# Kernel optimization log

Measured on AMD Instinct MI355X. Metric: run time of the kernel, lower is better.

## Reference

```python
import jax, jax.numpy as jnp
import numpy as np
import itertools

F = 20        # field_size
D = 16        # embedding_size / output_dims
H = 2         # num_hash
NB = 500000   # num_buckets
B = 4096      # batch
NI = F * (F - 1) // 2  # 190 pairwise interactions


def _interact_indexes(field_size):
    # For each field i, indices of the C(F,2) combinations that contain i -> [F, F-1]
    combos = list(itertools.combinations(range(field_size), 2))
    idx = [[j for j, c in enumerate(combos) if i in c] for i in range(field_size)]
    return np.asarray(idx, dtype=np.int32)


def setup_inputs() -> dict:
    key = jax.random.key(0)
    k0, k1, k2, k3, k4, k5 = jax.random.split(key, 6)
    return {
        "origin_embeddings": jax.random.normal(k0, (B, F, D), jnp.float32),
        "codebook": jax.random.normal(k1, (NB, D), jnp.float32) * 0.01,
        "W_transform": jax.random.normal(k2, (H * D, D), jnp.float32) * 0.05,
        "senet_w1": jax.random.normal(k3, (F * D, F * D), jnp.float32) * 0.02,
        "senet_w2": jax.random.normal(k4, (F * D, NI), jnp.float32) * 0.02,
        # Precomputed hash bucket ids (stands in for the StrongHash of string tokens)
        "hash_idx": jax.random.randint(k5, (H, B, NI), 0, NB, dtype=jnp.int32),
        "interact_indexes": jnp.asarray(_interact_indexes(F)),
    }


def reference(origin_embeddings, codebook, W_transform, senet_w1, senet_w2, hash_idx, interact_indexes):
    b = origin_embeddings.shape[0]
    # multi-hash codebook gathers (hash-share: one codebook): [H, B, NI, D]
    gathered = codebook[hash_idx]
    # merge_mode='concat' over hash functions -> [B, NI, H*D]
    emb = jnp.concatenate([gathered[i] for i in range(gathered.shape[0])], axis=-1)
    # hash_merge_final_transform: Dense(output_dims, no bias) -> [B, NI, D]
    emb = jnp.einsum('bne,ed->bnd', emb, W_transform)
    # SENET (bit squeeze, ratio 1.0, vector excitation, no activation) over origin embeddings
    z = origin_embeddings.reshape(b, -1)          # [B, F*D]
    w = (z @ senet_w1) @ senet_w2                 # [B, NI]
    # gather each field's interactions and weighted-sum ('senetsum')
    field_emb = emb[:, interact_indexes]          # [B, F, F-1, D]
    field_w = w[:, interact_indexes][..., None]   # [B, F, F-1, 1]
    out = jnp.sum(field_emb * field_w, axis=-2)   # [B, F, D]
    return out
```

## Files before the change

### kernel.cpp

```cpp
#include <hip/hip_runtime.h>

#define FF 20
#define NI 190
#define NIP 192
#define BB 4096
#define FD 320

__global__ __launch_bounds__(192) void k_w12(const float* __restrict__ w1,
                                             const float* __restrict__ w2,
                                             float* __restrict__ W12p) {
    __shared__ float srow[FD];
    int r = blockIdx.x;
    for (int j = threadIdx.x; j < FD; j += 192) srow[j] = w1[r * FD + j];
    __syncthreads();
    int c = threadIdx.x;
    float acc = 0.f;
    if (c < NI) {
        for (int k = 0; k < FD; ++k) acc += srow[k] * w2[k * NI + c];
    }
    W12p[r * NIP + c] = acc;
}

__global__ __launch_bounds__(256) void k_w(const float* __restrict__ z,
                                           const float* __restrict__ W12p,
                                           float* __restrict__ wout) {
    __shared__ float zT[32][68];
    __shared__ float Ws[32][64];
    int b0 = blockIdx.x * 64;
    int c0 = blockIdx.y * 64;
    int t = threadIdx.x;
    int tr = t >> 4, tc = t & 15;
    float acc[4][4];
#pragma unroll
    for (int i = 0; i < 4; ++i)
#pragma unroll
        for (int j = 0; j < 4; ++j) acc[i][j] = 0.f;

    for (int k0 = 0; k0 < FD; k0 += 32) {
#pragma unroll
        for (int s = 0; s < 2; ++s) {
            int task = t + s * 256;
            int row = task >> 3, ch = task & 7;
            float4 v = *(const float4*)&z[(b0 + row) * FD + k0 + ch * 4];
            zT[ch * 4 + 0][row] = v.x;
            zT[ch * 4 + 1][row] = v.y;
            zT[ch * 4 + 2][row] = v.z;
            zT[ch * 4 + 3][row] = v.w;
        }
#pragma unroll
        for (int s = 0; s < 2; ++s) {
            int task = t + s * 256;
            int kr = task >> 4, cq = task & 15;
            *(float4*)&Ws[kr][cq * 4] = *(const float4*)&W12p[(k0 + kr) * NIP + c0 + cq * 4];
        }
        __syncthreads();
#pragma unroll
        for (int k = 0; k < 32; ++k) {
            float4 zb = *(const float4*)&zT[k][tr * 4];
            float4 wv = *(const float4*)&Ws[k][tc * 4];
            float zz[4] = {zb.x, zb.y, zb.z, zb.w};
            float ww[4] = {wv.x, wv.y, wv.z, wv.w};
#pragma unroll
            for (int i = 0; i < 4; ++i)
#pragma unroll
                for (int j = 0; j < 4; ++j) acc[i][j] += zz[i] * ww[j];
        }
        __syncthreads();
    }
#pragma unroll
    for (int i = 0; i < 4; ++i) {
        float4 v = make_float4(acc[i][0], acc[i][1], acc[i][2], acc[i][3]);
        *(float4*)&wout[(b0 + tr * 4 + i) * NIP + c0 + tc * 4] = v;
    }
}

#define SA(f, h, d) ((f) * 33 + (h) * 16 + (d))
__global__ __launch_bounds__(320) void k_main(const float* __restrict__ cb,
                                              const float* __restrict__ Wt,
                                              const int* __restrict__ hidx,
                                              const int* __restrict__ iidx,
                                              const float* __restrict__ wbuf,
                                              float* __restrict__ out) {
    __shared__ int s_i0[NI], s_i1[NI];
    __shared__ float s_w[NI];
    __shared__ int s_plist[FF * 19];
    __shared__ float s_W[32 * 16];
    __shared__ float s_acc[19 * 33 + 2 * 16 + 16];

    int t = threadIdx.x;
    int b = blockIdx.x;

    if (t < NI) {
        s_i0[t] = hidx[b * NI + t];
        s_i1[t] = hidx[(BB + b) * NI + t];
        s_w[t] = wbuf[b * NIP + t];
    }
    for (int j = t; j < FF * 19; j += 320) s_plist[j] = iidx[j];
    for (int j = t; j < 512; j += 320) s_W[j] = Wt[j];
    __syncthreads();

    int f = t >> 4, d = t & 15;
    const int* pl = &s_plist[f * 19];
    float a0 = 0.f, a1 = 0.f;
#pragma unroll
    for (int j = 0; j < 19; ++j) {
        int p = pl[j];
        float wv = s_w[p];
        a0 += wv * cb[s_i0[p] * 16 + d];
        a1 += wv * cb[s_i1[p] * 16 + d];
    }
    s_acc[SA(f, 0, d)] = a0;
    s_acc[SA(f, 1, d)] = a1;
    __syncthreads();

    float r = 0.f;
#pragma unroll
    for (int k = 0; k < 16; ++k) {
        r += s_acc[SA(f, 0, k)] * s_W[k * 16 + d];
        r += s_acc[SA(f, 1, k)] * s_W[(16 + k) * 16 + d];
    }
    out[b * FD + t] = r;
}

extern "C" void kernel_launch(void* const* d_in, const int* in_sizes, int n_in,
                              void* d_out, int out_size, void* d_ws, size_t ws_size,
                              hipStream_t stream) {
    const float* origin = (const float*)d_in[0];
    const float* cb     = (const float*)d_in[1];
    const float* Wt     = (const float*)d_in[2];
    const float* w1     = (const float*)d_in[3];
    const float* w2     = (const float*)d_in[4];
    const int*   hidx   = (const int*)d_in[5];
    const int*   iidx   = (const int*)d_in[6];
    float* out = (float*)d_out;

    float* W12p = (float*)d_ws;
    float* wbuf = W12p + FD * NIP;

    k_w12<<<FD, 192, 0, stream>>>(w1, w2, W12p);
    dim3 gw(BB / 64, 3);
    k_w<<<gw, 256, 0, stream>>>(origin, W12p, wbuf);
    k_main<<<BB, 320, 0, stream>>>(cb, Wt, hidx, iidx, wbuf, out);
}
```

Measured before the change: 144.8 us.

## Process four batch rows per block with float4 codebook gathers

Each block of the main kernel now handles four batch rows, and each thread covers one quarter of a field's 16-wide embedding. Codebook rows are read as float4, so the per-element gather turns into vectorised 16-byte loads. The transform matmul reads W from shared memory as float4 and stores its output as float4. This cuts the number of gather instructions and amortises the per-block setup (interaction list, W) over more rows, at the cost of fewer blocks and lower thread-level parallelism per row.

```diff
diff --git a/kernel.cpp b/kernel.cpp
--- a/kernel.cpp
+++ b/kernel.cpp
@@ -5,6 +5,7 @@
 #define NIP 192
 #define BB 4096
 #define FD 320
+#define BPB 4
 
 __global__ __launch_bounds__(192) void k_w12(const float* __restrict__ w1,
                                              const float* __restrict__ w2,
@@ -74,52 +75,75 @@
     }
 }
 
-#define SA(f, h, d) ((f) * 33 + (h) * 16 + (d))
-__global__ __launch_bounds__(320) void k_main(const float* __restrict__ cb,
-                                              const float* __restrict__ Wt,
-                                              const int* __restrict__ hidx,
-                                              const int* __restrict__ iidx,
-                                              const float* __restrict__ wbuf,
-                                              float* __restrict__ out) {
-    __shared__ int s_i0[NI], s_i1[NI];
-    __shared__ float s_w[NI];
+#define SAC(bl, f, h, k) ((((bl) * FF + (f)) * 2 + (h)) * 17 + (k))
+__global__ __launch_bounds__(320, 4) void k_main(const float* __restrict__ cb,
+                                                 const float* __restrict__ Wt,
+                                                 const int* __restrict__ hidx,
+                                                 const int* __restrict__ iidx,
+                                                 const float* __restrict__ wbuf,
+                                                 float* __restrict__ out) {
+    __shared__ int s_i0[BPB][NI], s_i1[BPB][NI];
+    __shared__ float s_w[BPB][NI];
     __shared__ int s_plist[FF * 19];
     __shared__ float s_W[32 * 16];
-    __shared__ float s_acc[19 * 33 + 2 * 16 + 16];
+    __shared__ float s_acc[SAC(BPB - 1, FF - 1, 1, 16) + 1];
 
     int t = threadIdx.x;
-    int b = blockIdx.x;
+    int b0 = blockIdx.x * BPB;
 
-    if (t < NI) {
-        s_i0[t] = hidx[b * NI + t];
-        s_i1[t] = hidx[(BB + b) * NI + t];
-        s_w[t] = wbuf[b * NIP + t];
+#pragma unroll
+    for (int bl = 0; bl < BPB; ++bl) {
+        if (t < NI) {
+            s_i0[bl][t] = hidx[(b0 + bl) * NI + t];
+            s_i1[bl][t] = hidx[(BB + b0 + bl) * NI + t];
+            s_w[bl][t] = wbuf[(b0 + bl) * NIP + t];
+        }
     }
     for (int j = t; j < FF * 19; j += 320) s_plist[j] = iidx[j];
     for (int j = t; j < 512; j += 320) s_W[j] = Wt[j];
     __syncthreads();
 
-    int f = t >> 4, d = t & 15;
+    int bl = t / 80;
+    int r = t % 80;
+    int f = r >> 2, dq = r & 3;
+
+    const float4* cb4 = (const float4*)cb;
     const int* pl = &s_plist[f * 19];
-    float a0 = 0.f, a1 = 0.f;
+    float4 a0 = make_float4(0.f, 0.f, 0.f, 0.f);
+    float4 a1 = make_float4(0.f, 0.f, 0.f, 0.f);
 #pragma unroll
     for (int j = 0; j < 19; ++j) {
         int p = pl[j];
-        float wv = s_w[p];
-        a0 += wv * cb[s_i0[p] * 16 + d];
-        a1 += wv * cb[s_i1[p] * 16 + d];
+        float wv = s_w[bl][p];
+        float4 v0 = cb4[s_i0[bl][p] * 4 + dq];
+        float4 v1 = cb4[s_i1[bl][p] * 4 + dq];
+        a0.x += wv * v0.x; a0.y += wv * v0.y; a0.z += wv * v0.z; a0.w += wv * v0.w;
+        a1.x += wv * v1.x; a1.y += wv * v1.y; a1.z += wv * v1.z; a1.w += wv * v1.w;
     }
-    s_acc[SA(f, 0, d)] = a0;
-    s_acc[SA(f, 1, d)] = a1;
+    s_acc[SAC(bl, f, 0, dq * 4 + 0)] = a0.x;
+    s_acc[SAC(bl, f, 0, dq * 4 + 1)] = a0.y;
+    s_acc[SAC(bl, f, 0, dq * 4 + 2)] = a0.z;
+    s_acc[SAC(bl, f, 0, dq * 4 + 3)] = a0.w;
+    s_acc[SAC(bl, f, 1, dq * 4 + 0)] = a1.x;
+    s_acc[SAC(bl, f, 1, dq * 4 + 1)] = a1.y;
+    s_acc[SAC(bl, f, 1, dq * 4 + 2)] = a1.z;
+    s_acc[SAC(bl, f, 1, dq * 4 + 3)] = a1.w;
     __syncthreads();
 
-    float r = 0.f;
+    float4 rr = make_float4(0.f, 0.f, 0.f, 0.f);
 #pragma unroll
     for (int k = 0; k < 16; ++k) {
-        r += s_acc[SA(f, 0, k)] * s_W[k * 16 + d];
-        r += s_acc[SA(f, 1, k)] * s_W[(16 + k) * 16 + d];
+        float c0 = s_acc[SAC(bl, f, 0, k)];
+        float4 wv = *(const float4*)&s_W[k * 16 + dq * 4];
+        rr.x += c0 * wv.x; rr.y += c0 * wv.y; rr.z += c0 * wv.z; rr.w += c0 * wv.w;
     }
-    out[b * FD + t] = r;
+#pragma unroll
+    for (int k = 0; k < 16; ++k) {
+        float c1 = s_acc[SAC(bl, f, 1, k)];
+        float4 wv = *(const float4*)&s_W[(16 + k) * 16 + dq * 4];
+        rr.x += c1 * wv.x; rr.y += c1 * wv.y; rr.z += c1 * wv.z; rr.w += c1 * wv.w;
+    }
+    *(float4*)&out[(b0 + bl) * FD + f * 16 + dq * 4] = rr;
 }
 
 extern "C" void kernel_launch(void* const* d_in, const int* in_sizes, int n_in,
@@ -140,5 +164,5 @@
     k_w12<<<FD, 192, 0, stream>>>(w1, w2, W12p);
     dim3 gw(BB / 64, 3);
     k_w<<<gw, 256, 0, stream>>>(origin, W12p, wbuf);
-    k_main<<<BB, 320, 0, stream>>>(cb, Wt, hidx, iidx, wbuf, out);
+    k_main<<<BB / BPB, 320, 0, stream>>>(cb, Wt, hidx, iidx, wbuf, out);
 }
```

New measurement: 151.5 us. +4.7%, slower.

## Vectorize codebook gathers as float4 and split interaction sum across thread groups

Applied to the files above, without the earlier changes.

The main kernel now has each thread load codebook rows as float4 (four dims per thread). It splits the 19 interactions of each field across four thread groups whose partial sums are reduced in shared memory. The final projection is done by 80 threads writing float4 outputs. This targets fewer, wider random gather transactions with more loads in flight per thread. The cost is an extra reduction pass, an extra barrier, and idle threads in the last stage, plus an occupancy hint in the launch bounds.

```diff
diff --git a/kernel.cpp b/kernel.cpp
--- a/kernel.cpp
+++ b/kernel.cpp
@@ -74,18 +74,18 @@
     }
 }
 
-#define SA(f, h, d) ((f) * 33 + (h) * 16 + (d))
-__global__ __launch_bounds__(320) void k_main(const float* __restrict__ cb,
-                                              const float* __restrict__ Wt,
-                                              const int* __restrict__ hidx,
-                                              const int* __restrict__ iidx,
-                                              const float* __restrict__ wbuf,
-                                              float* __restrict__ out) {
+#define SAC(jg, f, h, k) ((((jg) * FF + (f)) * 2 + (h)) * 17 + (k))
+__global__ __launch_bounds__(320, 6) void k_main(const float* __restrict__ cb,
+                                                 const float* __restrict__ Wt,
+                                                 const int* __restrict__ hidx,
+                                                 const int* __restrict__ iidx,
+                                                 const float* __restrict__ wbuf,
+                                                 float* __restrict__ out) {
     __shared__ int s_i0[NI], s_i1[NI];
     __shared__ float s_w[NI];
     __shared__ int s_plist[FF * 19];
     __shared__ float s_W[32 * 16];
-    __shared__ float s_acc[19 * 33 + 2 * 16 + 16];
+    __shared__ float s_acc[4 * FF * 2 * 17];
 
     int t = threadIdx.x;
     int b = blockIdx.x;
@@ -99,27 +99,66 @@
     for (int j = t; j < 512; j += 320) s_W[j] = Wt[j];
     __syncthreads();
 
-    int f = t >> 4, d = t & 15;
+    int jg = t / 80;
+    int r = t % 80;
+    int f = r >> 2, dq = r & 3;
+
+    const float4* cb4 = (const float4*)cb;
     const int* pl = &s_plist[f * 19];
-    float a0 = 0.f, a1 = 0.f;
+    float4 a0 = make_float4(0.f, 0.f, 0.f, 0.f);
+    float4 a1 = make_float4(0.f, 0.f, 0.f, 0.f);
 #pragma unroll
-    for (int j = 0; j < 19; ++j) {
-        int p = pl[j];
-        float wv = s_w[p];
-        a0 += wv * cb[s_i0[p] * 16 + d];
-        a1 += wv * cb[s_i1[p] * 16 + d];
+    for (int jj = 0; jj < 5; ++jj) {
+        int j = jg * 5 + jj;
+        if (j < 19) {
+            int p = pl[j];
+            float wv = s_w[p];
+            float4 v0 = cb4[s_i0[p] * 4 + dq];
+            float4 v1 = cb4[s_i1[p] * 4 + dq];
+            a0.x += wv * v0.x; a0.y += wv * v0.y; a0.z += wv * v0.z; a0.w += wv * v0.w;
+            a1.x += wv * v1.x; a1.y += wv * v1.y; a1.z += wv * v1.z; a1.w += wv * v1.w;
+        }
     }
-    s_acc[SA(f, 0, d)] = a0;
-    s_acc[SA(f, 1, d)] = a1;
+    s_acc[SAC(jg, f, 0, dq * 4 + 0)] = a0.x;
+    s_acc[SAC(jg, f, 0, dq * 4 + 1)] = a0.y;
+    s_acc[SAC(jg, f, 0, dq * 4 + 2)] = a0.z;
+    s_acc[SAC(jg, f, 0, dq * 4 + 3)] = a0.w;
+    s_acc[SAC(jg, f, 1, dq * 4 + 0)] = a1.x;
+    s_acc[SAC(jg, f, 1, dq * 4 + 1)] = a1.y;
+    s_acc[SAC(jg, f, 1, dq * 4 + 2)] = a1.z;
+    s_acc[SAC(jg, f, 1, dq * 4 + 3)] = a1.w;
     __syncthreads();
 
-    float r = 0.f;
 #pragma unroll
-    for (int k = 0; k < 16; ++k) {
-        r += s_acc[SA(f, 0, k)] * s_W[k * 16 + d];
-        r += s_acc[SA(f, 1, k)] * s_W[(16 + k) * 16 + d];
+    for (int h = 0; h < 2; ++h) {
+#pragma unroll
+        for (int c = 0; c < 4; ++c) {
+            int k = dq * 4 + c;
+            if (jg == 0) {
+                s_acc[SAC(0, f, h, k)] += s_acc[SAC(1, f, h, k)] +
+                                          s_acc[SAC(2, f, h, k)] +
+                                          s_acc[SAC(3, f, h, k)];
+            }
+        }
     }
-    out[b * FD + t] = r;
+    __syncthreads();
+
+    if (t < 80) {
+        float4 rr = make_float4(0.f, 0.f, 0.f, 0.f);
+#pragma unroll
+        for (int k = 0; k < 16; ++k) {
+            float c0 = s_acc[SAC(0, f, 0, k)];
+            float4 wv = *(const float4*)&s_W[k * 16 + dq * 4];
+            rr.x += c0 * wv.x; rr.y += c0 * wv.y; rr.z += c0 * wv.z; rr.w += c0 * wv.w;
+        }
+#pragma unroll
+        for (int k = 0; k < 16; ++k) {
+            float c1 = s_acc[SAC(0, f, 1, k)];
+            float4 wv = *(const float4*)&s_W[(16 + k) * 16 + dq * 4];
+            rr.x += c1 * wv.x; rr.y += c1 * wv.y; rr.z += c1 * wv.z; rr.w += c1 * wv.w;
+        }
+        *(float4*)&out[b * FD + f * 16 + dq * 4] = rr;
+    }
 }
 
 extern "C" void kernel_launch(void* const* d_in, const int* in_sizes, int n_in,
```

Measured after the change: 146.0 us (median of 2 runs). About the same (+0.8%).
